# Kernel optimization log

Hardware: AMD Instinct MI355X
Metric: run time of the kernel (lower is better)

## Reference

```python
import jax, jax.numpy as jnp
import numpy as np

INPUT_DIM = 24
HIDDEN = 128
NUM_LAYERS = 3
OUTPUT_DIM = 1


def _lstm_layer(x, Wih, Whh, bih, bhh):
    """Single LSTM layer, PyTorch gate order (i, f, g, o). x: [B,T,D] -> [B,T,H]."""
    B = x.shape[0]
    H = Whh.shape[1]
    # Precompute input projections for all timesteps at once: [B,T,4H]
    xg = jnp.einsum('btd,gd->btg', x, Wih) + bih
    xg = jnp.swapaxes(xg, 0, 1)  # [T,B,4H]
    h0 = jnp.zeros((B, H), x.dtype)
    c0 = jnp.zeros((B, H), x.dtype)

    def step(carry, xt):
        h, c = carry
        gates = xt + h @ Whh.T + bhh  # [B,4H]
        i, f, g, o = jnp.split(gates, 4, axis=-1)
        i = jax.nn.sigmoid(i)
        f = jax.nn.sigmoid(f)
        g = jnp.tanh(g)
        o = jax.nn.sigmoid(o)
        c = f * c + i * g
        h = o * jnp.tanh(c)
        return (h, c), h

    _, hs = jax.lax.scan(step, (h0, c0), xg)  # hs: [T,B,H]
    return jnp.swapaxes(hs, 0, 1)  # [B,T,H]


def setup_inputs() -> dict:
    key = jax.random.key(0)
    ks = jax.random.split(key, 16)
    B, T = 2048, 256
    s = 0.05
    inp = {
        'x': jax.random.normal(ks[0], (B, T, INPUT_DIM), dtype=jnp.float32),
    }
    dims_in = [INPUT_DIM, HIDDEN, HIDDEN]
    for l in range(NUM_LAYERS):
        inp[f'Wih{l}'] = jax.random.normal(ks[1 + 4 * l], (4 * HIDDEN, dims_in[l]), dtype=jnp.float32) * s
        inp[f'Whh{l}'] = jax.random.normal(ks[2 + 4 * l], (4 * HIDDEN, HIDDEN), dtype=jnp.float32) * s
        inp[f'bih{l}'] = jax.random.normal(ks[3 + 4 * l], (4 * HIDDEN,), dtype=jnp.float32) * s
        inp[f'bhh{l}'] = jax.random.normal(ks[4 + 4 * l], (4 * HIDDEN,), dtype=jnp.float32) * s
    inp['Wfc'] = jax.random.normal(ks[13], (OUTPUT_DIM, HIDDEN), dtype=jnp.float32) * s
    inp['bfc'] = jax.random.normal(ks[14], (OUTPUT_DIM,), dtype=jnp.float32) * s
    return inp


def reference(x, Wih0, Whh0, bih0, bhh0, Wih1, Whh1, bih1, bhh1,
              Wih2, Whh2, bih2, bhh2, Wfc, bfc):
    # 3 stacked LSTM layers (dropout inactive in eval mode), zero initial state.
    h = _lstm_layer(x, Wih0, Whh0, bih0, bhh0)
    h = _lstm_layer(h, Wih1, Whh1, bih1, bhh1)
    h = _lstm_layer(h, Wih2, Whh2, bih2, bhh2)
    # Linear projection of the final timestep: [B,1]
    return h[:, -1, :] @ Wfc.T + bfc
```

## Files before the change

### kernel.cpp

```cpp
#include <hip/hip_runtime.h>

#define T_STEPS 256
#define BATCH   2048
#define HID     128
#define ROWS    8

typedef short short8  __attribute__((ext_vector_type(8)));
typedef short short4v __attribute__((ext_vector_type(4)));
typedef float float4v __attribute__((ext_vector_type(4)));

template<bool B> struct BoolC { static constexpr bool value = B; };

__device__ __forceinline__ unsigned short f2bf(float f) {
    unsigned int u = __builtin_bit_cast(unsigned int, f);
    u += 0x7fffu + ((u >> 16) & 1u);
    return (unsigned short)(u >> 16);
}
__device__ __forceinline__ float bf2f(unsigned short b) {
    unsigned int u = ((unsigned int)b) << 16;
    return __builtin_bit_cast(float, u);
}

#if __has_builtin(__builtin_amdgcn_exp2f)
#define EXP2F(x) __builtin_amdgcn_exp2f(x)
#else
#define EXP2F(x) exp2f(x)
#endif
__device__ __forceinline__ float sigf(float x) {
    return __builtin_amdgcn_rcpf(1.0f + EXP2F(x * -1.442695041f));
}
__device__ __forceinline__ float tanh_fast(float x) {
    return 2.0f * __builtin_amdgcn_rcpf(1.0f + EXP2F(x * -2.885390082f)) - 1.0f;
}

__device__ __forceinline__ void block_sync_lds() {
    asm volatile("s_waitcnt lgkmcnt(0)" ::: "memory");
    __builtin_amdgcn_s_barrier();
    __builtin_amdgcn_sched_barrier(0);
}

__device__ __forceinline__ int lposH(int row, int off) {
    return row * 256 + (off ^ ((row & 7) << 4));
}
__device__ __forceinline__ int lposX(int row, int off) {
    return row * 256 + (off ^ ((row & 7) << 4));
}
__device__ __forceinline__ int lposX0(int row, int off) {
    return row * 64 + (off ^ ((row & 3) << 4));
}

__device__ __forceinline__ short8 load_w8(const float* __restrict__ p) {
    float4v a = *reinterpret_cast<const float4v*>(p);
    float4v b = *reinterpret_cast<const float4v*>(p + 4);
    short8 r;
    r[0] = (short)f2bf(a[0]); r[1] = (short)f2bf(a[1]);
    r[2] = (short)f2bf(a[2]); r[3] = (short)f2bf(a[3]);
    r[4] = (short)f2bf(b[0]); r[5] = (short)f2bf(b[1]);
    r[6] = (short)f2bf(b[2]); r[7] = (short)f2bf(b[3]);
    return r;
}

#define LDS_BYTES 12288

template<bool IS_L0, bool WRITE_H, bool FINAL>
__device__ __forceinline__ void lstm_phase(
    unsigned char* a_lds,
    const float* __restrict__ x0,
    const float* __restrict__ Wih,
    const float* __restrict__ Whh,
    const float* __restrict__ bih,
    const float* __restrict__ bhh,
    unsigned short* __restrict__ hbuf,
    const float* __restrict__ Wfc,
    const float* __restrict__ bfc,
    float* __restrict__ out,
    const int tid, const int b0)
{
    constexpr int XKS = IS_L0 ? 1 : 4;
    constexpr int XRB = IS_L0 ? 64 : 256;
    constexpr int HB  = ROWS * 256;
    constexpr int XB  = 16 * XRB;
    const int XS0 = 2 * HB, XS1 = 2 * HB + XB;

    const int lane = tid & 63;
    const int wv   = tid >> 6;

    const int t16   = lane & 15;
    const int kgrp8 = (lane >> 4) * 8;
    const int jcol  = 16 * wv + t16;
    const int row0  = ((lane >> 4) & 1) * 4 + ((lane >> 5) & 1) * 2;

    const int g2   = t16 >> 2;
    const int hrow = ((g2 & 1) << 2) | ((g2 >> 1) << 1) | (t16 & 1);
    int aoffH[4];
    #pragma unroll
    for (int ks = 0; ks < 4; ++ks)
        aoffH[ks] = lposH(hrow, ks * 64 + kgrp8 * 2);
    int aoffX[XKS];
    #pragma unroll
    for (int s = 0; s < XKS; ++s)
        aoffX[s] = IS_L0 ? lposX0(t16, kgrp8 * 2)
                         : lposX(t16, s * 64 + kgrp8 * 2);

    const int hwoff0 = lposH(row0,     2 * jcol);
    const int hwoff1 = lposH(row0 + 1, 2 * jcol);

    const int srow4 = tid >> 6, scol4 = tid & 63;
    const int hroff4 = lposH(srow4, scol4 * 4);
    const size_t sgoff4 = (size_t)(b0 + srow4) * HID + scol4 * 2;

    const int sar = tid >> 5, sc8 = tid & 31;
    const int sb  = (sar & 1) | (((sar >> 3) & 1) << 1) | (((sar >> 2) & 1) << 2);
    const int ss  = (sar >> 1) & 1;
    const int xwoff = lposX(sar, sc8 * 8);
    const size_t xgrow = (size_t)(b0 + sb) * HID + sc8 * 4;
    const bool xvalid = tid < 384;
    const int ar0 = xvalid ? tid / 24 : 0, xc = xvalid ? tid % 24 : 0;
    const int xb_ = (ar0 & 1) | (((ar0 >> 3) & 1) << 1) | (((ar0 >> 2) & 1) << 2);
    const int xs  = (ar0 >> 1) & 1;
    const int xw0off = lposX0(ar0, xc * 2);
    const size_t x0row = (size_t)(b0 + xb_) * (T_STEPS * 24) + xc;

    short8 wfh[4][4], wfx[4][XKS];
    float  bias[4];
    #pragma unroll
    for (int q = 0; q < 4; ++q) {
        const int n = 128 * q + jcol;
        bias[q] = bih[n] + bhh[n];
        #pragma unroll
        for (int ks = 0; ks < 4; ++ks)
            wfh[q][ks] = load_w8(Whh + n * 128 + ks * 32 + kgrp8);
        if (IS_L0) {
            if (kgrp8 < 24) wfx[q][0] = load_w8(Wih + n * 24 + kgrp8);
            else            { short8 z = {0,0,0,0,0,0,0,0}; wfx[q][0] = z; }
        } else {
            #pragma unroll
            for (int s = 0; s < 4; ++s)
                wfx[q][s] = load_w8(Wih + n * 128 + s * 32 + kgrp8);
        }
    }

    {
        short8 z = {0,0,0,0,0,0,0,0};
        #pragma unroll
        for (int i = 0; i < 2; ++i) {
            const int a = tid * 16 + i * 8192;
            if (a < LDS_BYTES)
                *reinterpret_cast<short8*>(&a_lds[a]) = z;
        }
    }
    __syncthreads();

    short4v xpre = {0, 0, 0, 0};
    float   xpref = 0.f;
    if (!IS_L0) {
        short4v v = *reinterpret_cast<const short4v*>(
            &hbuf[(size_t)(0 + ss) * (BATCH * HID) + xgrow]);
        *reinterpret_cast<short4v*>(&a_lds[XS0 + xwoff]) = v;
        xpre = *reinterpret_cast<const short4v*>(
            &hbuf[(size_t)(2 + ss) * (BATCH * HID) + xgrow]);
    } else if (xvalid) {
        float v = x0[x0row + (size_t)(0 + xs) * 24];
        *reinterpret_cast<unsigned short*>(&a_lds[XS0 + xw0off]) = f2bf(v);
        xpref = x0[x0row + (size_t)(2 + xs) * 24];
    }
    __syncthreads();

    float4v xacc[4];
    #pragma unroll
    for (int q = 0; q < 4; ++q)
        xacc[q] = float4v{bias[q], bias[q], bias[q], bias[q]};
    {
        short8 xa[XKS];
        #pragma unroll
        for (int s = 0; s < XKS; ++s)
            xa[s] = *reinterpret_cast<const short8*>(&a_lds[XS0 + aoffX[s]]);
        #pragma unroll
        for (int s = 0; s < XKS; ++s)
            #pragma unroll
            for (int q = 0; q < 4; ++q)
                xacc[q] = __builtin_amdgcn_mfma_f32_16x16x32_bf16(xa[s], wfx[q][s], xacc[q], 0, 0, 0);
    }

    float creg[2] = {0.f, 0.f};

    auto do_step = [&](int t, auto ODDC) {
        constexpr bool ODD = decltype(ODDC)::value;
        const int rb = ODD ? HB : 0;
        const int wb = ODD ? 0 : HB;
        short8 hva[4];
        #pragma unroll
        for (int ks = 0; ks < 4; ++ks)
            hva[ks] = *reinterpret_cast<const short8*>(&a_lds[rb + aoffH[ks]]);
        short8 xa[XKS];
        const bool do_x = ODD && (t + 1 < T_STEPS);
        if (do_x) {
            const int xrb_ = ((((t + 1) >> 1) & 1) ? XS1 : XS0);
            #pragma unroll
            for (int s = 0; s < XKS; ++s)
                xa[s] = *reinterpret_cast<const short8*>(&a_lds[xrb_ + aoffX[s]]);
        }
        float4v acc[4];
        #pragma unroll
        for (int q = 0; q < 4; ++q) {
            const float a = ODD ? xacc[q][2] : xacc[q][0];
            const float b = ODD ? xacc[q][3] : xacc[q][1];
            acc[q] = float4v{a, b, a, b};
        }
        if (WRITE_H && t > 0) {
            unsigned int hv = *reinterpret_cast<const unsigned int*>(&a_lds[rb + hroff4]);
            *reinterpret_cast<unsigned int*>(
                &hbuf[(size_t)(t - 1) * (BATCH * HID) + sgoff4]) = hv;
        }
        if constexpr (!ODD) {
            const int xsb = ((((t >> 1) & 1) ^ 1) ? XS1 : XS0);
            if (!IS_L0) {
                if (t + 2 + ss < T_STEPS)
                    *reinterpret_cast<short4v*>(&a_lds[xsb + xwoff]) = xpre;
            } else if (xvalid && (t + 2 + xs < T_STEPS))
                *reinterpret_cast<unsigned short*>(&a_lds[xsb + xw0off]) = f2bf(xpref);
        } else {
            if (!IS_L0) {
                if (t + 3 + ss < T_STEPS)
                    xpre = *reinterpret_cast<const short4v*>(
                        &hbuf[(size_t)(t + 3 + ss) * (BATCH * HID) + xgrow]);
            } else if (xvalid && (t + 3 + xs < T_STEPS))
                xpref = x0[x0row + (size_t)(t + 3 + xs) * 24];
        }
        __builtin_amdgcn_s_setprio(1);
        #pragma unroll
        for (int ks = 0; ks < 4; ++ks)
            #pragma unroll
            for (int q = 0; q < 4; ++q)
                acc[q] = __builtin_amdgcn_mfma_f32_16x16x32_bf16(hva[ks], wfh[q][ks], acc[q], 0, 0, 0);
        if (do_x) {
            #pragma unroll
            for (int q = 0; q < 4; ++q)
                xacc[q] = float4v{bias[q], bias[q], bias[q], bias[q]};
            #pragma unroll
            for (int s = 0; s < XKS; ++s)
                #pragma unroll
                for (int q = 0; q < 4; ++q)
                    xacc[q] = __builtin_amdgcn_mfma_f32_16x16x32_bf16(xa[s], wfx[q][s], xacc[q], 0, 0, 0);
        }
        __builtin_amdgcn_s_setprio(0);
        const float c0 = sigf(acc[1][0]) * creg[0] + sigf(acc[0][0]) * tanh_fast(acc[2][0]);
        const float c1 = sigf(acc[1][1]) * creg[1] + sigf(acc[0][1]) * tanh_fast(acc[2][1]);
        creg[0] = c0;  creg[1] = c1;
        const float h0 = sigf(acc[3][0]) * tanh_fast(c0);
        const float h1 = sigf(acc[3][1]) * tanh_fast(c1);
        unsigned int packed;
        asm("v_cvt_pk_bf16_f32 %0, %1, %2" : "=v"(packed) : "v"(h0), "v"(h1));
        *reinterpret_cast<unsigned short*>(&a_lds[wb + hwoff0]) =
            (unsigned short)(packed & 0xffffu);
        *reinterpret_cast<unsigned short*>(&a_lds[wb + hwoff1]) =
            (unsigned short)(packed >> 16);
        block_sync_lds();
    };

    for (int th = 0; th < T_STEPS / 2; ++th) {
        do_step(2 * th,     BoolC<false>{});
        do_step(2 * th + 1, BoolC<true>{});
    }
    if (WRITE_H) {
        unsigned int hv = *reinterpret_cast<const unsigned int*>(&a_lds[hroff4]);
        *reinterpret_cast<unsigned int*>(
            &hbuf[(size_t)(T_STEPS - 1) * (BATCH * HID) + sgoff4]) = hv;
    }
    if (FINAL && tid < 128) {
        const int r = tid >> 4, seg = tid & 15;
        float s = 0.f;
        #pragma unroll
        for (int k = 0; k < 8; ++k) {
            const int j = seg * 8 + k;
            s += bf2f(*reinterpret_cast<const unsigned short*>(&a_lds[lposH(r, 2 * j)]))
                 * Wfc[j];
        }
        #pragma unroll
        for (int off = 8; off >= 1; off >>= 1) s += __shfl_xor(s, off);
        if (seg == 0) out[b0 + r] = s + bfc[0];
    }
}

__global__ __launch_bounds__(512, 2)
void lstm3(const float* __restrict__ x0,
           const float* __restrict__ Wih0, const float* __restrict__ Whh0,
           const float* __restrict__ bih0, const float* __restrict__ bhh0,
           const float* __restrict__ Wih1, const float* __restrict__ Whh1,
           const float* __restrict__ bih1, const float* __restrict__ bhh1,
           const float* __restrict__ Wih2, const float* __restrict__ Whh2,
           const float* __restrict__ bih2, const float* __restrict__ bhh2,
           const float* __restrict__ Wfc,  const float* __restrict__ bfc,
           unsigned short* __restrict__ hbuf, float* __restrict__ out)
{
    __shared__ __attribute__((aligned(16))) unsigned char a_lds[LDS_BYTES];
    const int tid = threadIdx.x;
    const int b0  = blockIdx.x * ROWS;

    lstm_phase<true,  true,  false>(a_lds, x0, Wih0, Whh0, bih0, bhh0, hbuf,
                                    nullptr, nullptr, nullptr, tid, b0);
    __syncthreads();
    lstm_phase<false, true,  false>(a_lds, nullptr, Wih1, Whh1, bih1, bhh1, hbuf,
                                    nullptr, nullptr, nullptr, tid, b0);
    __syncthreads();
    lstm_phase<false, false, true >(a_lds, nullptr, Wih2, Whh2, bih2, bhh2, hbuf,
                                    Wfc, bfc, out, tid, b0);
}

extern "C" void kernel_launch(void* const* d_in, const int* in_sizes, int n_in,
                              void* d_out, int out_size, void* d_ws, size_t ws_size,
                              hipStream_t stream) {
    (void)in_sizes; (void)n_in; (void)out_size; (void)ws_size;
    const float* x    = (const float*)d_in[0];
    const float* Wih0 = (const float*)d_in[1];
    const float* Whh0 = (const float*)d_in[2];
    const float* bih0 = (const float*)d_in[3];
    const float* bhh0 = (const float*)d_in[4];
    const float* Wih1 = (const float*)d_in[5];
    const float* Whh1 = (const float*)d_in[6];
    const float* bih1 = (const float*)d_in[7];
    const float* bhh1 = (const float*)d_in[8];
    const float* Wih2 = (const float*)d_in[9];
    const float* Whh2 = (const float*)d_in[10];
    const float* bih2 = (const float*)d_in[11];
    const float* bhh2 = (const float*)d_in[12];
    const float* Wfc  = (const float*)d_in[13];
    const float* bfc  = (const float*)d_in[14];
    float* out = (float*)d_out;
    unsigned short* hbuf = (unsigned short*)d_ws;

    dim3 grid(BATCH / ROWS), block(512);
    lstm3<<<grid, block, 0, stream>>>(x, Wih0, Whh0, bih0, bhh0,
                                      Wih1, Whh1, bih1, bhh1,
                                      Wih2, Whh2, bih2, bhh2,
                                      Wfc, bfc, hbuf, out);
}
```

Baseline: 586.0 us.

## Split input-projection MFMAs across step pairs and specialize wave roles for I/O

The input-projection MFMA work for the next step pair is now spread evenly over both the even and odd recurrent steps, using ping-pong xgA/xgB accumulators. Previously all of it sat on odd steps. Global traffic is also divided by thread half: threads below 256 store h to global with 8-byte writes, and the upper 256 threads prefetch the next layer input with wider 16-byte or float2 loads into a deeper x staging pipeline. The aim is to balance per-step critical-path latency and cut the number of memory instructions. The cost is more accumulator registers, and the loop is unrolled by four.

Measured after the change: 599.9 us. 1.02x slower.

```diff
diff --git a/kernel.cpp b/kernel.cpp
--- a/kernel.cpp
+++ b/kernel.cpp
@@ -4,12 +4,10 @@
 #define BATCH   2048
 #define HID     128
 #define ROWS    8
+#define BH      (BATCH * HID)
 
 typedef short short8  __attribute__((ext_vector_type(8)));
-typedef short short4v __attribute__((ext_vector_type(4)));
 typedef float float4v __attribute__((ext_vector_type(4)));
-
-template<bool B> struct BoolC { static constexpr bool value = B; };
 
 __device__ __forceinline__ unsigned short f2bf(float f) {
     unsigned int u = __builtin_bit_cast(unsigned int, f);
@@ -105,21 +103,19 @@
     const int hwoff0 = lposH(row0,     2 * jcol);
     const int hwoff1 = lposH(row0 + 1, 2 * jcol);
 
-    const int srow4 = tid >> 6, scol4 = tid & 63;
-    const int hroff4 = lposH(srow4, scol4 * 4);
-    const size_t sgoff4 = (size_t)(b0 + srow4) * HID + scol4 * 2;
-
-    const int sar = tid >> 5, sc8 = tid & 31;
+    const int sh_row = (tid >> 5) & 7, sh_c8 = tid & 31;
+    const int hroff8 = lposH(sh_row, sh_c8 * 8);
+    const size_t sgoff8 = (size_t)(b0 + sh_row) * HID + sh_c8 * 4;
+
+    const int tid2 = tid & 255;
+    const int sar = tid2 >> 4, sc16 = tid2 & 15;
     const int sb  = (sar & 1) | (((sar >> 3) & 1) << 1) | (((sar >> 2) & 1) << 2);
     const int ss  = (sar >> 1) & 1;
-    const int xwoff = lposX(sar, sc8 * 8);
-    const size_t xgrow = (size_t)(b0 + sb) * HID + sc8 * 4;
-    const bool xvalid = tid < 384;
-    const int ar0 = xvalid ? tid / 24 : 0, xc = xvalid ? tid % 24 : 0;
-    const int xb_ = (ar0 & 1) | (((ar0 >> 3) & 1) << 1) | (((ar0 >> 2) & 1) << 2);
-    const int xs  = (ar0 >> 1) & 1;
-    const int xw0off = lposX0(ar0, xc * 2);
-    const size_t x0row = (size_t)(b0 + xb_) * (T_STEPS * 24) + xc;
+    const int xwoff = lposX(sar, sc16 * 16);
+    const size_t xgrow = (size_t)(b0 + sb) * HID + sc16 * 8;
+    const bool xvalid = (sc16 < 12);
+    const int xw0off = lposX0(sar, sc16 * 4);
+    const size_t x0row = (size_t)(b0 + sb) * (T_STEPS * 24) + sc16 * 2;
 
     short8 wfh[4][4], wfx[4][XKS];
     float  bias[4];
@@ -151,25 +147,34 @@
     }
     __syncthreads();
 
-    short4v xpre = {0, 0, 0, 0};
-    float   xpref = 0.f;
-    if (!IS_L0) {
-        short4v v = *reinterpret_cast<const short4v*>(
-            &hbuf[(size_t)(0 + ss) * (BATCH * HID) + xgrow]);
-        *reinterpret_cast<short4v*>(&a_lds[XS0 + xwoff]) = v;
-        xpre = *reinterpret_cast<const short4v*>(
-            &hbuf[(size_t)(2 + ss) * (BATCH * HID) + xgrow]);
-    } else if (xvalid) {
-        float v = x0[x0row + (size_t)(0 + xs) * 24];
-        *reinterpret_cast<unsigned short*>(&a_lds[XS0 + xw0off]) = f2bf(v);
-        xpref = x0[x0row + (size_t)(2 + xs) * 24];
+    short8 xpre = {0,0,0,0,0,0,0,0};
+    float2 xpf  = {0.f, 0.f};
+    if (tid >= 256) {
+        if (!IS_L0) {
+            short8 v0 = *reinterpret_cast<const short8*>(&hbuf[(size_t)(0 + ss) * BH + xgrow]);
+            short8 v1 = *reinterpret_cast<const short8*>(&hbuf[(size_t)(2 + ss) * BH + xgrow]);
+            *reinterpret_cast<short8*>(&a_lds[XS0 + xwoff]) = v0;
+            *reinterpret_cast<short8*>(&a_lds[XS1 + xwoff]) = v1;
+            xpre = *reinterpret_cast<const short8*>(&hbuf[(size_t)(4 + ss) * BH + xgrow]);
+        } else if (xvalid) {
+            float2 a = *reinterpret_cast<const float2*>(&x0[x0row + (size_t)(0 + ss) * 24]);
+            float2 b = *reinterpret_cast<const float2*>(&x0[x0row + (size_t)(2 + ss) * 24]);
+            unsigned int pa, pb;
+            asm("v_cvt_pk_bf16_f32 %0, %1, %2" : "=v"(pa) : "v"(a.x), "v"(a.y));
+            asm("v_cvt_pk_bf16_f32 %0, %1, %2" : "=v"(pb) : "v"(b.x), "v"(b.y));
+            *reinterpret_cast<unsigned int*>(&a_lds[XS0 + xw0off]) = pa;
+            *reinterpret_cast<unsigned int*>(&a_lds[XS1 + xw0off]) = pb;
+            xpf = *reinterpret_cast<const float2*>(&x0[x0row + (size_t)(4 + ss) * 24]);
+        }
     }
     __syncthreads();
 
-    float4v xacc[4];
+    float4v xgA[4], xgB[4];
     #pragma unroll
-    for (int q = 0; q < 4; ++q)
-        xacc[q] = float4v{bias[q], bias[q], bias[q], bias[q]};
+    for (int q = 0; q < 4; ++q) {
+        xgA[q] = float4v{bias[q], bias[q], bias[q], bias[q]};
+        xgB[q] = float4v{bias[q], bias[q], bias[q], bias[q]};
+    }
     {
         short8 xa[XKS];
         #pragma unroll
@@ -179,71 +184,13 @@
         for (int s = 0; s < XKS; ++s)
             #pragma unroll
             for (int q = 0; q < 4; ++q)
-                xacc[q] = __builtin_amdgcn_mfma_f32_16x16x32_bf16(xa[s], wfx[q][s], xacc[q], 0, 0, 0);
-    }
+                xgA[q] = __builtin_amdgcn_mfma_f32_16x16x32_bf16(xa[s], wfx[q][s], xgA[q], 0, 0, 0);
+    }
+    block_sync_lds();
 
     float creg[2] = {0.f, 0.f};
 
-    auto do_step = [&](int t, auto ODDC) {
-        constexpr bool ODD = decltype(ODDC)::value;
-        const int rb = ODD ? HB : 0;
-        const int wb = ODD ? 0 : HB;
-        short8 hva[4];
-        #pragma unroll
-        for (int ks = 0; ks < 4; ++ks)
-            hva[ks] = *reinterpret_cast<const short8*>(&a_lds[rb + aoffH[ks]]);
-        short8 xa[XKS];
-        const bool do_x = ODD && (t + 1 < T_STEPS);
-        if (do_x) {
-            const int xrb_ = ((((t + 1) >> 1) & 1) ? XS1 : XS0);
-            #pragma unroll
-            for (int s = 0; s < XKS; ++s)
-                xa[s] = *reinterpret_cast<const short8*>(&a_lds[xrb_ + aoffX[s]]);
-        }
-        float4v acc[4];
-        #pragma unroll
-        for (int q = 0; q < 4; ++q) {
-            const float a = ODD ? xacc[q][2] : xacc[q][0];
-            const float b = ODD ? xacc[q][3] : xacc[q][1];
-            acc[q] = float4v{a, b, a, b};
-        }
-        if (WRITE_H && t > 0) {
-            unsigned int hv = *reinterpret_cast<const unsigned int*>(&a_lds[rb + hroff4]);
-            *reinterpret_cast<unsigned int*>(
-                &hbuf[(size_t)(t - 1) * (BATCH * HID) + sgoff4]) = hv;
-        }
-        if constexpr (!ODD) {
-            const int xsb = ((((t >> 1) & 1) ^ 1) ? XS1 : XS0);
-            if (!IS_L0) {
-                if (t + 2 + ss < T_STEPS)
-                    *reinterpret_cast<short4v*>(&a_lds[xsb + xwoff]) = xpre;
-            } else if (xvalid && (t + 2 + xs < T_STEPS))
-                *reinterpret_cast<unsigned short*>(&a_lds[xsb + xw0off]) = f2bf(xpref);
-        } else {
-            if (!IS_L0) {
-                if (t + 3 + ss < T_STEPS)
-                    xpre = *reinterpret_cast<const short4v*>(
-                        &hbuf[(size_t)(t + 3 + ss) * (BATCH * HID) + xgrow]);
-            } else if (xvalid && (t + 3 + xs < T_STEPS))
-                xpref = x0[x0row + (size_t)(t + 3 + xs) * 24];
-        }
-        __builtin_amdgcn_s_setprio(1);
-        #pragma unroll
-        for (int ks = 0; ks < 4; ++ks)
-            #pragma unroll
-            for (int q = 0; q < 4; ++q)
-                acc[q] = __builtin_amdgcn_mfma_f32_16x16x32_bf16(hva[ks], wfh[q][ks], acc[q], 0, 0, 0);
-        if (do_x) {
-            #pragma unroll
-            for (int q = 0; q < 4; ++q)
-                xacc[q] = float4v{bias[q], bias[q], bias[q], bias[q]};
-            #pragma unroll
-            for (int s = 0; s < XKS; ++s)
-                #pragma unroll
-                for (int q = 0; q < 4; ++q)
-                    xacc[q] = __builtin_amdgcn_mfma_f32_16x16x32_bf16(xa[s], wfx[q][s], xacc[q], 0, 0, 0);
-        }
-        __builtin_amdgcn_s_setprio(0);
+    auto cell_write = [&](float4v (&acc)[4], int wb) {
         const float c0 = sigf(acc[1][0]) * creg[0] + sigf(acc[0][0]) * tanh_fast(acc[2][0]);
         const float c1 = sigf(acc[1][1]) * creg[1] + sigf(acc[0][1]) * tanh_fast(acc[2][1]);
         creg[0] = c0;  creg[1] = c1;
@@ -255,17 +202,130 @@
             (unsigned short)(packed & 0xffffu);
         *reinterpret_cast<unsigned short*>(&a_lds[wb + hwoff1]) =
             (unsigned short)(packed >> 16);
+    };
+
+    auto stepE = [&](int t, float4v (&cons)[4], float4v (&bld)[4],
+                     const int XRD, const int XST) {
+        short8 hva[4];
+        #pragma unroll
+        for (int ks = 0; ks < 4; ++ks)
+            hva[ks] = *reinterpret_cast<const short8*>(&a_lds[0 + aoffH[ks]]);
+        short8 xa0, xa1;
+        if constexpr (!IS_L0) {
+            xa0 = *reinterpret_cast<const short8*>(&a_lds[XRD + aoffX[0]]);
+            xa1 = *reinterpret_cast<const short8*>(&a_lds[XRD + aoffX[1]]);
+        } else {
+            xa0 = *reinterpret_cast<const short8*>(&a_lds[XRD + aoffX[0]]);
+        }
+        float4v acc[4];
+        #pragma unroll
+        for (int q = 0; q < 4; ++q) {
+            const float a = cons[q][0], b = cons[q][1];
+            acc[q] = float4v{a, b, a, b};
+        }
+        if (tid < 256) {
+            if (WRITE_H && t > 0) {
+                int2 hv = *reinterpret_cast<const int2*>(&a_lds[0 + hroff8]);
+                *reinterpret_cast<int2*>(&hbuf[(size_t)(t - 1) * BH + sgoff8]) = hv;
+            }
+        } else {
+            if constexpr (!IS_L0) {
+                *reinterpret_cast<short8*>(&a_lds[XST + xwoff]) = xpre;
+            } else {
+                if (xvalid) {
+                    unsigned int p;
+                    asm("v_cvt_pk_bf16_f32 %0, %1, %2" : "=v"(p) : "v"(xpf.x), "v"(xpf.y));
+                    *reinterpret_cast<unsigned int*>(&a_lds[XST + xw0off]) = p;
+                }
+            }
+        }
+        __builtin_amdgcn_s_setprio(1);
+        #pragma unroll
+        for (int ks = 0; ks < 4; ++ks)
+            #pragma unroll
+            for (int q = 0; q < 4; ++q)
+                acc[q] = __builtin_amdgcn_mfma_f32_16x16x32_bf16(hva[ks], wfh[q][ks], acc[q], 0, 0, 0);
+        #pragma unroll
+        for (int q = 0; q < 4; ++q)
+            bld[q] = float4v{bias[q], bias[q], bias[q], bias[q]};
+        if constexpr (!IS_L0) {
+            #pragma unroll
+            for (int q = 0; q < 4; ++q)
+                bld[q] = __builtin_amdgcn_mfma_f32_16x16x32_bf16(xa0, wfx[q][0], bld[q], 0, 0, 0);
+            #pragma unroll
+            for (int q = 0; q < 4; ++q)
+                bld[q] = __builtin_amdgcn_mfma_f32_16x16x32_bf16(xa1, wfx[q][1], bld[q], 0, 0, 0);
+        } else {
+            #pragma unroll
+            for (int q = 0; q < 4; ++q)
+                bld[q] = __builtin_amdgcn_mfma_f32_16x16x32_bf16(xa0, wfx[q][0], bld[q], 0, 0, 0);
+        }
+        __builtin_amdgcn_s_setprio(0);
+        cell_write(acc, HB);
         block_sync_lds();
     };
 
-    for (int th = 0; th < T_STEPS / 2; ++th) {
-        do_step(2 * th,     BoolC<false>{});
-        do_step(2 * th + 1, BoolC<true>{});
-    }
-    if (WRITE_H) {
-        unsigned int hv = *reinterpret_cast<const unsigned int*>(&a_lds[hroff4]);
-        *reinterpret_cast<unsigned int*>(
-            &hbuf[(size_t)(T_STEPS - 1) * (BATCH * HID) + sgoff4]) = hv;
+    auto stepO = [&](int t, float4v (&cons)[4], float4v (&bld)[4],
+                     const int XRD) {
+        short8 hva[4];
+        #pragma unroll
+        for (int ks = 0; ks < 4; ++ks)
+            hva[ks] = *reinterpret_cast<const short8*>(&a_lds[HB + aoffH[ks]]);
+        short8 xa2, xa3;
+        if constexpr (!IS_L0) {
+            xa2 = *reinterpret_cast<const short8*>(&a_lds[XRD + aoffX[2]]);
+            xa3 = *reinterpret_cast<const short8*>(&a_lds[XRD + aoffX[3]]);
+        }
+        float4v acc[4];
+        #pragma unroll
+        for (int q = 0; q < 4; ++q) {
+            const float a = cons[q][2], b = cons[q][3];
+            acc[q] = float4v{a, b, a, b};
+        }
+        if (tid < 256) {
+            if (WRITE_H) {
+                int2 hv = *reinterpret_cast<const int2*>(&a_lds[HB + hroff8]);
+                *reinterpret_cast<int2*>(&hbuf[(size_t)(t - 1) * BH + sgoff8]) = hv;
+            }
+        } else {
+            int tl = t + 5 + ss;
+            tl = (tl < T_STEPS) ? tl : (T_STEPS - 1);
+            if constexpr (!IS_L0) {
+                xpre = *reinterpret_cast<const short8*>(&hbuf[(size_t)tl * BH + xgrow]);
+            } else {
+                if (xvalid)
+                    xpf = *reinterpret_cast<const float2*>(&x0[x0row + (size_t)tl * 24]);
+            }
+        }
+        __builtin_amdgcn_s_setprio(1);
+        #pragma unroll
+        for (int ks = 0; ks < 4; ++ks)
+            #pragma unroll
+            for (int q = 0; q < 4; ++q)
+                acc[q] = __builtin_amdgcn_mfma_f32_16x16x32_bf16(hva[ks], wfh[q][ks], acc[q], 0, 0, 0);
+        if constexpr (!IS_L0) {
+            #pragma unroll
+            for (int q = 0; q < 4; ++q)
+                bld[q] = __builtin_amdgcn_mfma_f32_16x16x32_bf16(xa2, wfx[q][2], bld[q], 0, 0, 0);
+            #pragma unroll
+            for (int q = 0; q < 4; ++q)
+                bld[q] = __builtin_amdgcn_mfma_f32_16x16x32_bf16(xa3, wfx[q][3], bld[q], 0, 0, 0);
+        }
+        __builtin_amdgcn_s_setprio(0);
+        cell_write(acc, 0);
+        block_sync_lds();
+    };
+
+    for (int q4 = 0; q4 < T_STEPS / 4; ++q4) {
+        const int t0 = 4 * q4;
+        stepE(t0,     xgA, xgB, XS1, XS0);
+        stepO(t0 + 1, xgA, xgB, XS1);
+        stepE(t0 + 2, xgB, xgA, XS0, XS1);
+        stepO(t0 + 3, xgB, xgA, XS0);
+    }
+    if (WRITE_H && tid < 256) {
+        int2 hv = *reinterpret_cast<const int2*>(&a_lds[0 + hroff8]);
+        *reinterpret_cast<int2*>(&hbuf[(size_t)(T_STEPS - 1) * BH + sgoff8]) = hv;
     }
     if (FINAL && tid < 128) {
         const int r = tid >> 4, seg = tid & 15;
```
